# Performance work log

Hardware: AMD Instinct MI355X
Metric: run time of the kernel (lower is better)

## Reference

```python
import jax, jax.numpy as jnp
import numpy as np

EMBED = 256
HEADS = 8
HEAD_DIM = EMBED // HEADS
POOL = 2
H_FEAT = 64
W_FEAT = 64
SCALE = HEAD_DIM ** -0.5
POOL_COMP = float(np.log(POOL * POOL))  # log(pool_size^2) logit compensation


def setup_inputs() -> dict:
    key = jax.random.key(0)
    ks = jax.random.split(key, 11)
    B, Nq = 1, H_FEAT * W_FEAT          # 4096 query tokens (one frame)
    num_spatial = 4 * H_FEAT * W_FEAT   # 4 memory frames -> 16384 spatial tokens
    n_ptr = 64                          # object pointer tokens (not pooled)
    s = 1.0 / np.sqrt(EMBED)
    inp = {
        "q": jax.random.normal(ks[0], (B, Nq, EMBED), jnp.float32),
        "k": jax.random.normal(ks[1], (B, num_spatial + n_ptr, EMBED), jnp.float32),
        "v": jax.random.normal(ks[2], (B, num_spatial + n_ptr, EMBED), jnp.float32),
        "Wq": jax.random.normal(ks[3], (EMBED, EMBED), jnp.float32) * s,
        "bq": jax.random.normal(ks[4], (EMBED,), jnp.float32) * 0.01,
        "Wk": jax.random.normal(ks[5], (EMBED, EMBED), jnp.float32) * s,
        "bk": jax.random.normal(ks[6], (EMBED,), jnp.float32) * 0.01,
        "Wv": jax.random.normal(ks[7], (EMBED, EMBED), jnp.float32) * s,
        "bv": jax.random.normal(ks[8], (EMBED,), jnp.float32) * 0.01,
        "Wo": jax.random.normal(ks[9], (EMBED, EMBED), jnp.float32) * s,
        "bo": jax.random.normal(ks[10], (EMBED,), jnp.float32) * 0.01,
        "num_spatial_mem": num_spatial,
    }
    return inp


def _pool_spatial(tokens, num_spatial):
    """Avg-pool spatial tokens with POOLxPOOL windows; keep pointer tokens."""
    B, N, C = tokens.shape
    sp = tokens[:, :num_spatial, :]
    ptr = tokens[:, num_spatial:, :]
    frames = num_spatial // (H_FEAT * W_FEAT)
    hp, wp = H_FEAT // POOL, W_FEAT // POOL
    sp = sp.reshape(B, frames, hp, POOL, wp, POOL, C).mean(axis=(3, 5))
    sp = sp.reshape(B, frames * hp * wp, C)
    return jnp.concatenate([sp, ptr], axis=1), frames * hp * wp


def _heads(x):
    B, N, _ = x.shape
    return x.reshape(B, N, HEADS, HEAD_DIM).transpose(0, 2, 1, 3)  # (B,h,N,d)


def reference(q, k, v, Wq, bq, Wk, bk, Wv, bv, Wo, bo, num_spatial_mem):
    B, Nq, _ = q.shape
    qp = q @ Wq + bq
    k_pooled, n_sp_pooled = _pool_spatial(k, num_spatial_mem)
    v_pooled, _ = _pool_spatial(v, num_spatial_mem)
    kp = k_pooled @ Wk + bk
    vp = v_pooled @ Wv + bv
    qh, kh, vh = _heads(qp), _heads(kp), _heads(vp)
    logits = jnp.einsum('bhqd,bhkd->bhqk', qh, kh) * SCALE
    # additive bias on the pooled-key subset only
    logits = logits.at[..., :n_sp_pooled].add(POOL_COMP)
    attn = jax.nn.softmax(logits, axis=-1)
    out = jnp.einsum('bhqk,bhkd->bhqd', attn, vh)
    out = out.transpose(0, 2, 1, 3).reshape(B, Nq, EMBED)
    return out @ Wo + bo
```

## Files before the change

kernel.cpp:

```cpp
#include <hip/hip_runtime.h>
#include <hip/hip_bf16.h>
#include <cstdint>

#define NQ 4096
#define NK 4160
#define NSP 16384
#define E 256
#define HD 32
#define SC2E 0.2550348652937f
#define C2_SP  -12.426950408889634f
#define C2_PTR -14.426950408889634f

typedef __attribute__((ext_vector_type(4))) float f32x4;
typedef __attribute__((ext_vector_type(8))) __bf16 bf16x8;
typedef __attribute__((ext_vector_type(4))) __bf16 bf16x4;

__global__ __launch_bounds__(256) void wprep_kernel(
    const float* __restrict__ Wq, const float* __restrict__ Wk,
    const float* __restrict__ Wv, const float* __restrict__ Wo,
    __bf16* __restrict__ wthi, __bf16* __restrict__ wtlo)
{
  __shared__ float tl[32][33];
  const int b = blockIdx.x, t = threadIdx.x;
  const int wsel = b >> 6, tile = b & 63;
  const float* W = (wsel == 0) ? Wq : (wsel == 1) ? Wk : (wsel == 2) ? Wv : Wo;
  __bf16* oh = wthi + (size_t)wsel * 65536;
  __bf16* ol = wtlo + (size_t)wsel * 65536;
  const int tr = (tile >> 3) * 32, tc = (tile & 7) * 32;
  const int rr = t >> 3, cc = (t & 7) * 4;
  *(float4*)&tl[rr][cc] = *(const float4*)(W + (size_t)(tr + rr) * E + tc + cc);
  __syncthreads();
  bf16x4 hv, lv;
#pragma unroll
  for (int i = 0; i < 4; ++i) {
    float x = tl[cc + i][rr];
    __bf16 bh = (__bf16)x;
    hv[i] = bh;
    lv[i] = (__bf16)(x - (float)bh);
  }
  *(bf16x4*)(oh + (size_t)(tc + rr) * E + tr + cc) = hv;
  *(bf16x4*)(ol + (size_t)(tc + rr) * E + tr + cc) = lv;
}

template<int MODE>
__device__ __forceinline__ void qkv_body(
    const float* __restrict__ Xsrc, const __bf16* __restrict__ WTH,
    const float* __restrict__ bias, void* __restrict__ Y, int r0)
{
  __shared__ __bf16 Xs[16][264];
  const int t = threadIdx.x;

  {
    const int pr = t >> 4, f4 = t & 15;
    const int p = r0 + pr;
    float4 x[4];
    if (MODE == 0) {
      const float* src = Xsrc + (size_t)p * E + f4 * 4;
#pragma unroll
      for (int j = 0; j < 4; ++j) x[j] = *(const float4*)(src + j * 64);
    } else if (p < 4096) {
      const int fr = p >> 10, hp = (p >> 5) & 31, wp = p & 31;
      const float* src = Xsrc + (size_t)(fr * 4096 + hp * 128 + wp * 2) * E + f4 * 4;
#pragma unroll
      for (int j = 0; j < 4; ++j) {
        float4 a = *(const float4*)(src + j * 64);
        float4 b = *(const float4*)(src + j * 64 + E);
        float4 c = *(const float4*)(src + j * 64 + 64 * E);
        float4 d = *(const float4*)(src + j * 64 + 65 * E);
        x[j].x = 0.25f * (a.x + b.x + c.x + d.x);
        x[j].y = 0.25f * (a.y + b.y + c.y + d.y);
        x[j].z = 0.25f * (a.z + b.z + c.z + d.z);
        x[j].w = 0.25f * (a.w + b.w + c.w + d.w);
      }
    } else {
      const float* src = Xsrc + (size_t)(NSP + p - 4096) * E + f4 * 4;
#pragma unroll
      for (int j = 0; j < 4; ++j) x[j] = *(const float4*)(src + j * 64);
    }
#pragma unroll
    for (int j = 0; j < 4; ++j) {
      bf16x4 o;
      o[0] = (__bf16)x[j].x; o[1] = (__bf16)x[j].y;
      o[2] = (__bf16)x[j].z; o[3] = (__bf16)x[j].w;
      *(bf16x4*)&Xs[pr][f4 * 4 + j * 64] = o;
    }
  }
  __syncthreads();

  const int lane = t & 63, ql = lane & 15, g = lane >> 4;
  const int w = t >> 6, c0 = w * 64;
  const __bf16* wh0 = WTH + (size_t)(c0 + ql) * E + g * 8;

  f32x4 acc[4] = {};
#pragma unroll
  for (int k0 = 0; k0 < 8; ++k0) {
    bf16x8 a = *(const bf16x8*)&Xs[ql][g * 8 + k0 * 32];
#pragma unroll
    for (int j = 0; j < 4; ++j) {
      bf16x8 bh = *(const bf16x8*)(wh0 + (size_t)j * 16 * E + k0 * 32);
      if (MODE == 2) acc[j] = __builtin_amdgcn_mfma_f32_16x16x32_bf16(bh, a, acc[j], 0, 0, 0);
      else           acc[j] = __builtin_amdgcn_mfma_f32_16x16x32_bf16(a, bh, acc[j], 0, 0, 0);
    }
  }

  if (MODE == 0 || MODE == 1) {
    const int NN = (MODE == 0) ? NQ : NK;
#pragma unroll
    for (int j = 0; j < 4; ++j) {
      const int c = c0 + 16 * j + ql;
      const float bv = bias[c];
      const int hh = c >> 5, d = c & 31;
      __bf16* dst = (__bf16*)Y + (size_t)hh * NN * HD + d;
#pragma unroll
      for (int r = 0; r < 4; ++r) {
        const int n = r0 + g * 4 + r;
        float o = acc[j][r] + bv;
        if (MODE == 0) o *= SC2E;
        dst[(size_t)n * HD] = (__bf16)o;
      }
    }
  } else {
    const int n = r0 + ql;
    const int wi = n & 31;
    const int pos = ((wi & 15) >> 2) * 8 + (wi & 3) + 4 * ((wi >> 4) & 1);
    const size_t nb = (size_t)(n >> 5) * 32 + pos;
#pragma unroll
    for (int j = 0; j < 4; ++j)
#pragma unroll
      for (int r = 0; r < 4; ++r) {
        const int ch = c0 + 16 * j + g * 4 + r;
        const int hh = ch >> 5, d = ch & 31;
        ((__bf16*)Y)[(size_t)(hh * HD + d) * NK + nb] = (__bf16)(acc[j][r] + bias[ch]);
      }
  }
}

__global__ __launch_bounds__(256) void gemm_qkv(
    const float* __restrict__ q, const float* __restrict__ k, const float* __restrict__ v,
    const __bf16* __restrict__ wthi,
    const float* __restrict__ bq, const float* __restrict__ bk, const float* __restrict__ bv,
    __bf16* __restrict__ qb, __bf16* __restrict__ kb, __bf16* __restrict__ vtp)
{
  const int b = blockIdx.x;
  if (b < 256) {
    qkv_body<0>(q, wthi, bq, qb, b * 16);
  } else if (b < 516) {
    qkv_body<1>(k, wthi + 65536, bk, kb, (b - 256) * 16);
  } else {
    qkv_body<2>(v, wthi + 2 * 65536, bv, vtp, (b - 516) * 16);
  }
}

__global__ __launch_bounds__(256) void gemm_o(
    const __bf16* __restrict__ ahi, const __bf16* __restrict__ alo,
    const __bf16* __restrict__ WTH, const __bf16* __restrict__ WTL,
    const float* __restrict__ bias, float* __restrict__ out)
{
  const int r0 = blockIdx.x * 16;
  const int t = threadIdx.x;
  const int lane = t & 63, ql = lane & 15, g = lane >> 4;
  const int w = t >> 6, c0 = w * 64;

  const __bf16* xp  = ahi + (size_t)(r0 + ql) * E + g * 8;
  const __bf16* xlp = alo + (size_t)(r0 + ql) * E + g * 8;
  const __bf16* wh0 = WTH + (size_t)(c0 + ql) * E + g * 8;
  const __bf16* wl0 = WTL + (size_t)(c0 + ql) * E + g * 8;

  f32x4 acc[4] = {};
#pragma unroll
  for (int k0 = 0; k0 < 8; ++k0) {
    bf16x8 a  = *(const bf16x8*)(xp + k0 * 32);
    bf16x8 al = *(const bf16x8*)(xlp + k0 * 32);
#pragma unroll
    for (int j = 0; j < 4; ++j) {
      bf16x8 bh = *(const bf16x8*)(wh0 + (size_t)j * 16 * E + k0 * 32);
      bf16x8 bl = *(const bf16x8*)(wl0 + (size_t)j * 16 * E + k0 * 32);
      acc[j] = __builtin_amdgcn_mfma_f32_16x16x32_bf16(a,  bh, acc[j], 0, 0, 0);
      acc[j] = __builtin_amdgcn_mfma_f32_16x16x32_bf16(al, bh, acc[j], 0, 0, 0);
      acc[j] = __builtin_amdgcn_mfma_f32_16x16x32_bf16(a,  bl, acc[j], 0, 0, 0);
    }
  }
#pragma unroll
  for (int j = 0; j < 4; ++j) {
    const int c = c0 + 16 * j + ql;
    const float bv = bias[c];
#pragma unroll
    for (int r = 0; r < 4; ++r) {
      const int n = r0 + g * 4 + r;
      out[(size_t)n * E + c] = acc[j][r] + bv;
    }
  }
}

__global__ __launch_bounds__(512, 4) void attn_kernel(
    const __bf16* __restrict__ qb, const __bf16* __restrict__ kb,
    const __bf16* __restrict__ vtp, __bf16* __restrict__ ahi, __bf16* __restrict__ alo)
{
  __shared__ float OUT[4][64][36];
  __shared__ float LS[4][64];

  const int t = threadIdx.x;
  const int w = t >> 6, lane = t & 63;
  const int ql = lane & 15, g = lane >> 4;
  const int b = blockIdx.x;
  const int h = b & 7, qt = b >> 3;
  const int n0 = qt * 64;

  bf16x8 bq[4];
#pragma unroll
  for (int f = 0; f < 4; ++f)
    bq[f] = *(const bf16x8*)(qb + ((size_t)h * NQ + n0 + f * 16 + ql) * HD + g * 8);

  const int st = w * 16 + (w < 2 ? w : 2);
  const int nt = 16 + (w < 2 ? 1 : 0);

  const __bf16* kp = kb  + ((size_t)h * NK + st * 32 + ql) * HD + g * 8;
  const __bf16* vp = vtp + ((size_t)(h * HD) + ql) * NK + st * 32 + g * 8;
  const __bf16* vq = vp + (size_t)16 * NK;

  f32x4 o0[4] = {}, o1[4] = {};
  float ls[4] = {0.f, 0.f, 0.f, 0.f};

  bf16x8 kf0 = *(const bf16x8*)(kp);
  bf16x8 kf1 = *(const bf16x8*)(kp + 512);
  bf16x8 vf0 = *(const bf16x8*)(vp);
  bf16x8 vf1 = *(const bf16x8*)(vq);

#define TILE(C2V)                                                                   \
  _Pragma("unroll")                                                                 \
  for (int f = 0; f < 4; ++f) {                                                     \
    f32x4 s0 = __builtin_amdgcn_mfma_f32_16x16x32_bf16(kf0, bq[f], C2V, 0, 0, 0);   \
    f32x4 s1 = __builtin_amdgcn_mfma_f32_16x16x32_bf16(kf1, bq[f], C2V, 0, 0, 0);   \
    float e0 = __builtin_amdgcn_exp2f(s0[0]), e1 = __builtin_amdgcn_exp2f(s0[1]);   \
    float e2 = __builtin_amdgcn_exp2f(s0[2]), e3 = __builtin_amdgcn_exp2f(s0[3]);   \
    float e4 = __builtin_amdgcn_exp2f(s1[0]), e5 = __builtin_amdgcn_exp2f(s1[1]);   \
    float e6 = __builtin_amdgcn_exp2f(s1[2]), e7 = __builtin_amdgcn_exp2f(s1[3]);   \
    ls[f] += ((e0 + e1) + (e2 + e3)) + ((e4 + e5) + (e6 + e7));                     \
    bf16x8 p;                                                                       \
    p[0] = (__bf16)e0; p[1] = (__bf16)e1; p[2] = (__bf16)e2; p[3] = (__bf16)e3;     \
    p[4] = (__bf16)e4; p[5] = (__bf16)e5; p[6] = (__bf16)e6; p[7] = (__bf16)e7;     \
    o0[f] = __builtin_amdgcn_mfma_f32_16x16x32_bf16(p, vf0, o0[f], 0, 0, 0);        \
    o1[f] = __builtin_amdgcn_mfma_f32_16x16x32_bf16(p, vf1, o1[f], 0, 0, 0);        \
  }

  for (int it = 0; it < nt - 1; ++it) {
    bf16x8 nk0 = *(const bf16x8*)(kp + (size_t)(it + 1) * 1024);
    bf16x8 nk1 = *(const bf16x8*)(kp + (size_t)(it + 1) * 1024 + 512);
    bf16x8 nv0 = *(const bf16x8*)(vp + (size_t)(it + 1) * 32);
    bf16x8 nv1 = *(const bf16x8*)(vq + (size_t)(it + 1) * 32);
    const float c2 = (st + it < 128) ? C2_SP : C2_PTR;
    const f32x4 c2v = {c2, c2, c2, c2};
    TILE(c2v)
    kf0 = nk0; kf1 = nk1; vf0 = nv0; vf1 = nv1;
  }
  {
    const float c2 = (st + nt - 1 < 128) ? C2_SP : C2_PTR;
    const f32x4 c2v = {c2, c2, c2, c2};
    TILE(c2v)
  }
#undef TILE

#pragma unroll
  for (int f = 0; f < 4; ++f) {
    ls[f] += __shfl_xor(ls[f], 16);
    ls[f] += __shfl_xor(ls[f], 32);
  }

  if (w < 4) {
#pragma unroll
    for (int f = 0; f < 4; ++f) {
#pragma unroll
      for (int r = 0; r < 4; ++r) {
        OUT[w][f * 16 + g * 4 + r][ql]      = o0[f][r];
        OUT[w][f * 16 + g * 4 + r][16 + ql] = o1[f][r];
      }
      if (g == 0) LS[w][f * 16 + ql] = ls[f];
    }
  }
  __syncthreads();
  if (w >= 4) {
    const int w4 = w - 4;
#pragma unroll
    for (int f = 0; f < 4; ++f) {
#pragma unroll
      for (int r = 0; r < 4; ++r) {
        OUT[w4][f * 16 + g * 4 + r][ql]      += o0[f][r];
        OUT[w4][f * 16 + g * 4 + r][16 + ql] += o1[f][r];
      }
      if (g == 0) LS[w4][f * 16 + ql] += ls[f];
    }
  }
  __syncthreads();

  {
    const int q = t >> 3, d0 = (t & 7) * 4;
    f32x4 s = *(const f32x4*)&OUT[0][q][d0];
    float lsum = LS[0][q];
#pragma unroll
    for (int w2 = 1; w2 < 4; ++w2) {
      s += *(const f32x4*)&OUT[w2][q][d0];
      lsum += LS[w2][q];
    }
    const float inv = 1.0f / lsum;
    bf16x4 hv, lv;
#pragma unroll
    for (int i = 0; i < 4; ++i) {
      float o = s[i] * inv;
      __bf16 bh = (__bf16)o;
      hv[i] = bh;
      lv[i] = (__bf16)(o - (float)bh);
    }
    const size_t off = (size_t)(n0 + q) * E + h * HD + d0;
    *(bf16x4*)(ahi + off) = hv;
    *(bf16x4*)(alo + off) = lv;
  }
}

extern "C" void kernel_launch(void* const* d_in, const int* in_sizes, int n_in,
                              void* d_out, int out_size, void* d_ws, size_t ws_size,
                              hipStream_t stream)
{
  const float* q  = (const float*)d_in[0];
  const float* k  = (const float*)d_in[1];
  const float* v  = (const float*)d_in[2];
  const float* Wq = (const float*)d_in[3];
  const float* bq = (const float*)d_in[4];
  const float* Wk = (const float*)d_in[5];
  const float* bk = (const float*)d_in[6];
  const float* Wv = (const float*)d_in[7];
  const float* bv = (const float*)d_in[8];
  const float* Wo = (const float*)d_in[9];
  const float* bo = (const float*)d_in[10];
  float* out = (float*)d_out;

  char* wsp = (char*)d_ws;
  __bf16* wthi = (__bf16*)(wsp);
  __bf16* wtlo = (__bf16*)(wsp + 524288);
  __bf16* qbb  = (__bf16*)(wsp + 1048576);
  __bf16* kbb  = (__bf16*)(wsp + 3145728);
  __bf16* vtp  = (__bf16*)(wsp + 5275648);
  __bf16* ahi  = (__bf16*)(wsp + 7405568);
  __bf16* alo  = (__bf16*)(wsp + 9502720);

  wprep_kernel<<<256, 256, 0, stream>>>(Wq, Wk, Wv, Wo, wthi, wtlo);
  gemm_qkv<<<776, 256, 0, stream>>>(q, k, v, wthi, bq, bk, bv, qbb, kbb, vtp);
  attn_kernel<<<512, 512, 0, stream>>>(qbb, kbb, vtp, ahi, alo);
  gemm_o<<<256, 256, 0, stream>>>(ahi, alo, wthi + 3 * 65536, wtlo + 3 * 65536, bo, out);
}
```

Before: 69.98 us.

## Split attention keys across two blocks and merge partials in output GEMM

The attention kernel now splits the key range into two halves handled by separate blocks, doubling the grid to 1024 blocks. Each block writes unnormalised fp32 partial outputs and row sums to workspace. The output projection kernel adds the two partials, normalises, and does the hi/lo bf16 split before its MFMAs. The aim is more parallelism and occupancy in the attention stage, at the cost of extra fp32 global traffic. The merge relies on a fixed softmax offset rather than a running max, which is what the existing code already does.

```diff
diff --git a/kernel.cpp b/kernel.cpp
--- a/kernel.cpp
+++ b/kernel.cpp
@@ -152,7 +152,7 @@
 }
 
 __global__ __launch_bounds__(256) void gemm_o(
-    const __bf16* __restrict__ ahi, const __bf16* __restrict__ alo,
+    const float* __restrict__ oacc, const float* __restrict__ lsp,
     const __bf16* __restrict__ WTH, const __bf16* __restrict__ WTL,
     const float* __restrict__ bias, float* __restrict__ out)
 {
@@ -161,16 +161,30 @@
   const int lane = t & 63, ql = lane & 15, g = lane >> 4;
   const int w = t >> 6, c0 = w * 64;
 
-  const __bf16* xp  = ahi + (size_t)(r0 + ql) * E + g * 8;
-  const __bf16* xlp = alo + (size_t)(r0 + ql) * E + g * 8;
+  const float* o0p = oacc + (size_t)(r0 + ql) * E;
+  const float* o1p = o0p + (size_t)NQ * E;
+  const float* l0p = lsp + (size_t)(r0 + ql) * 8;
+  const float* l1p = l0p + (size_t)NQ * 8;
   const __bf16* wh0 = WTH + (size_t)(c0 + ql) * E + g * 8;
   const __bf16* wl0 = WTL + (size_t)(c0 + ql) * E + g * 8;
 
   f32x4 acc[4] = {};
 #pragma unroll
   for (int k0 = 0; k0 < 8; ++k0) {
-    bf16x8 a  = *(const bf16x8*)(xp + k0 * 32);
-    bf16x8 al = *(const bf16x8*)(xlp + k0 * 32);
+    const float inv = 1.0f / (l0p[k0] + l1p[k0]);
+    const int co = k0 * 32 + g * 8;
+    f32x4 xa = *(const f32x4*)(o0p + co)     + *(const f32x4*)(o1p + co);
+    f32x4 xb = *(const f32x4*)(o0p + co + 4) + *(const f32x4*)(o1p + co + 4);
+    bf16x8 a, al;
+#pragma unroll
+    for (int i = 0; i < 4; ++i) {
+      float x = xa[i] * inv;
+      __bf16 bh = (__bf16)x;
+      a[i] = bh; al[i] = (__bf16)(x - (float)bh);
+      float y = xb[i] * inv;
+      __bf16 bh2 = (__bf16)y;
+      a[4 + i] = bh2; al[4 + i] = (__bf16)(y - (float)bh2);
+    }
 #pragma unroll
     for (int j = 0; j < 4; ++j) {
       bf16x8 bh = *(const bf16x8*)(wh0 + (size_t)j * 16 * E + k0 * 32);
@@ -194,7 +208,7 @@
 
 __global__ __launch_bounds__(512, 4) void attn_kernel(
     const __bf16* __restrict__ qb, const __bf16* __restrict__ kb,
-    const __bf16* __restrict__ vtp, __bf16* __restrict__ ahi, __bf16* __restrict__ alo)
+    const __bf16* __restrict__ vtp, float* __restrict__ oacc, float* __restrict__ lsp)
 {
   __shared__ float OUT[4][64][36];
   __shared__ float LS[4][64];
@@ -203,7 +217,7 @@
   const int w = t >> 6, lane = t & 63;
   const int ql = lane & 15, g = lane >> 4;
   const int b = blockIdx.x;
-  const int h = b & 7, qt = b >> 3;
+  const int h = b & 7, part = (b >> 3) & 1, qt = b >> 4;
   const int n0 = qt * 64;
 
   bf16x8 bq[4];
@@ -211,8 +225,9 @@
   for (int f = 0; f < 4; ++f)
     bq[f] = *(const bf16x8*)(qb + ((size_t)h * NQ + n0 + f * 16 + ql) * HD + g * 8);
 
-  const int st = w * 16 + (w < 2 ? w : 2);
-  const int nt = 16 + (w < 2 ? 1 : 0);
+  const int stl = (w == 0) ? 0 : 9 + (w - 1) * 8;
+  const int nt  = (w == 0) ? 9 : 8;
+  const int st  = part * 65 + stl;
 
   const __bf16* kp = kb  + ((size_t)h * NK + st * 32 + ql) * HD + g * 8;
   const __bf16* vp = vtp + ((size_t)(h * HD) + ql) * NK + st * 32 + g * 8;
@@ -301,18 +316,10 @@
       s += *(const f32x4*)&OUT[w2][q][d0];
       lsum += LS[w2][q];
     }
-    const float inv = 1.0f / lsum;
-    bf16x4 hv, lv;
-#pragma unroll
-    for (int i = 0; i < 4; ++i) {
-      float o = s[i] * inv;
-      __bf16 bh = (__bf16)o;
-      hv[i] = bh;
-      lv[i] = (__bf16)(o - (float)bh);
-    }
-    const size_t off = (size_t)(n0 + q) * E + h * HD + d0;
-    *(bf16x4*)(ahi + off) = hv;
-    *(bf16x4*)(alo + off) = lv;
+    float* dst = oacc + ((size_t)part * NQ + n0 + q) * E + h * HD + d0;
+    *(f32x4*)dst = s;
+    if ((t & 7) == 0)
+      lsp[((size_t)part * NQ + n0 + q) * 8 + h] = lsum;
   }
 }
 
@@ -339,11 +346,11 @@
   __bf16* qbb  = (__bf16*)(wsp + 1048576);
   __bf16* kbb  = (__bf16*)(wsp + 3145728);
   __bf16* vtp  = (__bf16*)(wsp + 5275648);
-  __bf16* ahi  = (__bf16*)(wsp + 7405568);
-  __bf16* alo  = (__bf16*)(wsp + 9502720);
+  float*  oacc = (float*)(wsp + 7405568);
+  float*  lsp  = (float*)(wsp + 15794176);
 
   wprep_kernel<<<256, 256, 0, stream>>>(Wq, Wk, Wv, Wo, wthi, wtlo);
   gemm_qkv<<<776, 256, 0, stream>>>(q, k, v, wthi, bq, bk, bv, qbb, kbb, vtp);
-  attn_kernel<<<512, 512, 0, stream>>>(qbb, kbb, vtp, ahi, alo);
-  gemm_o<<<256, 256, 0, stream>>>(ahi, alo, wthi + 3 * 65536, wtlo + 3 * 65536, bo, out);
-}
+  attn_kernel<<<1024, 512, 0, stream>>>(qbb, kbb, vtp, oacc, lsp);
+  gemm_o<<<256, 256, 0, stream>>>(oacc, lsp, wthi + 3 * 65536, wtlo + 3 * 65536, bo, out);
+}
```

New measurement: 74.26 us. +6.1%, slower.

## Fuse output projection into attention kernel via per-head atomic accumulation

Applied to the files above, without the earlier changes.

Removes the separate output-projection GEMM kernel and the global round trip of the attention output's hi/lo bf16 split. Each attention block now multiplies its 64x32 head slice by the matching Wo rows using split-bf16 MFMAs and adds the partial result into the fp32 output with atomicAdd. The weight-prep kernel pre-fills the output with the bias. This saves one launch and the intermediate buffers, but adds 8-way atomic contention per output element and makes the summation order nondeterministic.

```diff
diff --git a/kernel.cpp b/kernel.cpp
--- a/kernel.cpp
+++ b/kernel.cpp
@@ -18,6 +18,7 @@
 __global__ __launch_bounds__(256) void wprep_kernel(
     const float* __restrict__ Wq, const float* __restrict__ Wk,
     const float* __restrict__ Wv, const float* __restrict__ Wo,
+    const float* __restrict__ bo, float* __restrict__ out,
     __bf16* __restrict__ wthi, __bf16* __restrict__ wtlo)
 {
   __shared__ float tl[32][33];
@@ -40,6 +41,11 @@
   }
   *(bf16x4*)(oh + (size_t)(tc + rr) * E + tr + cc) = hv;
   *(bf16x4*)(ol + (size_t)(tc + rr) * E + tr + cc) = lv;
+
+  const float bv = bo[t];
+#pragma unroll
+  for (int i = 0; i < 16; ++i)
+    out[(size_t)(b * 16 + i) * E + t] = bv;
 }
 
 template<int MODE>
@@ -151,53 +157,16 @@
   }
 }
 
-__global__ __launch_bounds__(256) void gemm_o(
-    const __bf16* __restrict__ ahi, const __bf16* __restrict__ alo,
-    const __bf16* __restrict__ WTH, const __bf16* __restrict__ WTL,
-    const float* __restrict__ bias, float* __restrict__ out)
-{
-  const int r0 = blockIdx.x * 16;
-  const int t = threadIdx.x;
-  const int lane = t & 63, ql = lane & 15, g = lane >> 4;
-  const int w = t >> 6, c0 = w * 64;
-
-  const __bf16* xp  = ahi + (size_t)(r0 + ql) * E + g * 8;
-  const __bf16* xlp = alo + (size_t)(r0 + ql) * E + g * 8;
-  const __bf16* wh0 = WTH + (size_t)(c0 + ql) * E + g * 8;
-  const __bf16* wl0 = WTL + (size_t)(c0 + ql) * E + g * 8;
-
-  f32x4 acc[4] = {};
-#pragma unroll
-  for (int k0 = 0; k0 < 8; ++k0) {
-    bf16x8 a  = *(const bf16x8*)(xp + k0 * 32);
-    bf16x8 al = *(const bf16x8*)(xlp + k0 * 32);
-#pragma unroll
-    for (int j = 0; j < 4; ++j) {
-      bf16x8 bh = *(const bf16x8*)(wh0 + (size_t)j * 16 * E + k0 * 32);
-      bf16x8 bl = *(const bf16x8*)(wl0 + (size_t)j * 16 * E + k0 * 32);
-      acc[j] = __builtin_amdgcn_mfma_f32_16x16x32_bf16(a,  bh, acc[j], 0, 0, 0);
-      acc[j] = __builtin_amdgcn_mfma_f32_16x16x32_bf16(al, bh, acc[j], 0, 0, 0);
-      acc[j] = __builtin_amdgcn_mfma_f32_16x16x32_bf16(a,  bl, acc[j], 0, 0, 0);
-    }
-  }
-#pragma unroll
-  for (int j = 0; j < 4; ++j) {
-    const int c = c0 + 16 * j + ql;
-    const float bv = bias[c];
-#pragma unroll
-    for (int r = 0; r < 4; ++r) {
-      const int n = r0 + g * 4 + r;
-      out[(size_t)n * E + c] = acc[j][r] + bv;
-    }
-  }
-}
-
 __global__ __launch_bounds__(512, 4) void attn_kernel(
     const __bf16* __restrict__ qb, const __bf16* __restrict__ kb,
-    const __bf16* __restrict__ vtp, __bf16* __restrict__ ahi, __bf16* __restrict__ alo)
+    const __bf16* __restrict__ vtp,
+    const __bf16* __restrict__ woh, const __bf16* __restrict__ wol,
+    float* __restrict__ out)
 {
   __shared__ float OUT[4][64][36];
   __shared__ float LS[4][64];
+  __shared__ __bf16 AH[64][40];
+  __shared__ __bf16 AL[64][40];
 
   const int t = threadIdx.x;
   const int w = t >> 6, lane = t & 63;
@@ -302,17 +271,43 @@
       lsum += LS[w2][q];
     }
     const float inv = 1.0f / lsum;
-    bf16x4 hv, lv;
 #pragma unroll
     for (int i = 0; i < 4; ++i) {
       float o = s[i] * inv;
       __bf16 bh = (__bf16)o;
-      hv[i] = bh;
-      lv[i] = (__bf16)(o - (float)bh);
-    }
-    const size_t off = (size_t)(n0 + q) * E + h * HD + d0;
-    *(bf16x4*)(ahi + off) = hv;
-    *(bf16x4*)(alo + off) = lv;
+      AH[q][d0 + i] = bh;
+      AL[q][d0 + i] = (__bf16)(o - (float)bh);
+    }
+  }
+  __syncthreads();
+
+  {
+    const __bf16* wohp = woh + (size_t)(w * 32 + ql) * E + h * 32 + g * 8;
+    const __bf16* wolp = wol + (size_t)(w * 32 + ql) * E + h * 32 + g * 8;
+    bf16x8 bh[2], bl[2];
+#pragma unroll
+    for (int j = 0; j < 2; ++j) {
+      bh[j] = *(const bf16x8*)(wohp + (size_t)j * 16 * E);
+      bl[j] = *(const bf16x8*)(wolp + (size_t)j * 16 * E);
+    }
+#pragma unroll
+    for (int f = 0; f < 4; ++f) {
+      bf16x8 a  = *(const bf16x8*)&AH[f * 16 + ql][g * 8];
+      bf16x8 al = *(const bf16x8*)&AL[f * 16 + ql][g * 8];
+#pragma unroll
+      for (int j = 0; j < 2; ++j) {
+        f32x4 acc = {0.f, 0.f, 0.f, 0.f};
+        acc = __builtin_amdgcn_mfma_f32_16x16x32_bf16(a,  bh[j], acc, 0, 0, 0);
+        acc = __builtin_amdgcn_mfma_f32_16x16x32_bf16(al, bh[j], acc, 0, 0, 0);
+        acc = __builtin_amdgcn_mfma_f32_16x16x32_bf16(a,  bl[j], acc, 0, 0, 0);
+        const int c = w * 32 + 16 * j + ql;
+#pragma unroll
+        for (int r = 0; r < 4; ++r) {
+          const int n = n0 + f * 16 + g * 4 + r;
+          atomicAdd(out + (size_t)n * E + c, acc[r]);
+        }
+      }
+    }
   }
 }
 
@@ -339,11 +334,9 @@
   __bf16* qbb  = (__bf16*)(wsp + 1048576);
   __bf16* kbb  = (__bf16*)(wsp + 3145728);
   __bf16* vtp  = (__bf16*)(wsp + 5275648);
-  __bf16* ahi  = (__bf16*)(wsp + 7405568);
-  __bf16* alo  = (__bf16*)(wsp + 9502720);
-
-  wprep_kernel<<<256, 256, 0, stream>>>(Wq, Wk, Wv, Wo, wthi, wtlo);
+
+  wprep_kernel<<<256, 256, 0, stream>>>(Wq, Wk, Wv, Wo, bo, out, wthi, wtlo);
   gemm_qkv<<<776, 256, 0, stream>>>(q, k, v, wthi, bq, bk, bv, qbb, kbb, vtp);
-  attn_kernel<<<512, 512, 0, stream>>>(qbb, kbb, vtp, ahi, alo);
-  gemm_o<<<256, 256, 0, stream>>>(ahi, alo, wthi + 3 * 65536, wtlo + 3 * 65536, bo, out);
-}
+  attn_kernel<<<512, 512, 0, stream>>>(qbb, kbb, vtp,
+                                       wthi + 3 * 65536, wtlo + 3 * 65536, out);
+}
```

Result: slower. 80.38 us (+14.9%).
